# Kernel tuning notes

Hardware: AMD Instinct MI355X
Metric: run time of the kernel (lower is better)

Reference implementation:

```python
import jax, jax.numpy as jnp
import numpy as np

HEADS = 16
HIDDEN = 1024
DH = HIDDEN // HEADS
EPS = 1e-6


def setup_inputs() -> dict:
    key = jax.random.key(0)
    ks = jax.random.split(key, 18)
    B, S, D, H = 8, 4096, HIDDEN, HEADS
    std = 0.02
    inp = {
        "x": jax.random.normal(ks[0], (B, S, D), dtype=jnp.float32),
        "mask": jnp.zeros((B, 1, S), dtype=jnp.float32),
        "Wq": std * jax.random.normal(ks[1], (D, D), dtype=jnp.float32),
        "bq": jnp.zeros((D,), jnp.float32),
        "Wk": std * jax.random.normal(ks[2], (D, D), dtype=jnp.float32),
        "bk": jnp.zeros((D,), jnp.float32),
        "Wv": std * jax.random.normal(ks[3], (D, D), dtype=jnp.float32),
        "bv": jnp.zeros((D,), jnp.float32),
        "Wa": std * jax.random.normal(ks[4], (D, H), dtype=jnp.float32),
        "ba": jnp.zeros((H,), jnp.float32),
        "Wb": std * jax.random.normal(ks[5], (D, H), dtype=jnp.float32),
        "bb": jnp.zeros((H,), jnp.float32),
        "Wu": std * jax.random.normal(ks[6], (D, D), dtype=jnp.float32),
        "bu": jnp.zeros((D,), jnp.float32),
        "Wo": std * jax.random.normal(ks[7], (D, D), dtype=jnp.float32),
        "bo": jnp.zeros((D,), jnp.float32),
        "ln_g": jnp.ones((D,), jnp.float32),
        "ln_b": jnp.zeros((D,), jnp.float32),
    }
    return inp


def reference(x, mask, Wq, bq, Wk, bk, Wv, bv, Wa, ba, Wb, bb, Wu, bu, Wo, bo, ln_g, ln_b):
    B, S, D = x.shape
    H, dh = HEADS, D // HEADS
    scale = (D / H) ** -0.5

    q = x @ Wq + bq  # [B,S,D]
    k = x @ Wk + bk
    v = x @ Wv + bv

    # alpha pooling of q
    ascore = jnp.swapaxes((q @ Wa + ba) * scale, 1, 2) + mask  # [B,H,S]
    aw = jax.nn.softmax(ascore, axis=-1)
    qh = q.reshape(B, S, H, dh)
    q_av = jnp.einsum("bhs,bshd->bhd", aw, qh).reshape(B, 1, D)  # global query

    p = k * q_av  # [B,S,D], broadcast over seq

    # beta pooling of p
    bscore = jnp.swapaxes((p @ Wb + bb) * scale, 1, 2) + mask  # [B,H,S]
    bw = jax.nn.softmax(bscore, axis=-1)
    ph = p.reshape(B, S, H, dh)
    p_av = jnp.einsum("bhs,bshd->bhd", bw, ph).reshape(B, 1, D)  # global key

    u = p_av * v  # [B,S,D]
    r = u @ Wu + bu
    attn_out = (r + q) @ Wo + bo

    y = x + attn_out  # residual (dropout is identity at inference)
    mu = jnp.mean(y, axis=-1, keepdims=True)
    var = jnp.mean(jnp.square(y - mu), axis=-1, keepdims=True)
    return (y - mu) * jax.lax.rsqrt(var + EPS) * ln_g + ln_b
```

## Files before the change

### kernel.cpp

```cpp
#include <hip/hip_runtime.h>

typedef unsigned short u16;
typedef __bf16 bf16x8 __attribute__((ext_vector_type(8)));
typedef float  f32x4  __attribute__((ext_vector_type(4)));

__device__ __forceinline__ float b2f(u16 u) {
    unsigned int v = ((unsigned int)u) << 16;
    return __builtin_bit_cast(float, v);
}
__device__ __forceinline__ u16 f2b(float f) {
    unsigned int v = __builtin_bit_cast(unsigned int, f);
    v += 0x7fffu + ((v >> 16) & 1u);
    return (u16)(v >> 16);
}

#define GLD16(gp, lp) __builtin_amdgcn_global_load_lds( \
    (const __attribute__((address_space(1))) void*)(gp), \
    (__attribute__((address_space(3))) void*)(lp), 16, 0, 0)


__global__ __launch_bounds__(256) void convert_x(const float* __restrict__ x,
                                                 u16* __restrict__ xb) {
    size_t i = ((size_t)blockIdx.x * 256 + threadIdx.x) * 8;
    float4 v0 = *(const float4*)(x + i);
    float4 v1 = *(const float4*)(x + i + 4);
    ushort4 o0, o1;
    o0.x = f2b(v0.x); o0.y = f2b(v0.y); o0.z = f2b(v0.z); o0.w = f2b(v0.w);
    o1.x = f2b(v1.x); o1.y = f2b(v1.y); o1.z = f2b(v1.z); o1.w = f2b(v1.w);
    *(ushort4*)(xb + i)     = o0;
    *(ushort4*)(xb + i + 4) = o1;
}

__global__ __launch_bounds__(256) void transpose_w(const float* __restrict__ W,
                                                   u16* __restrict__ Wt) {
    __shared__ float tile[64][65];
    int kt = (blockIdx.x & 15) * 64;
    int nt = (blockIdx.x >> 4) * 64;
    int tid = threadIdx.x;
    int r = tid >> 4, c4 = (tid & 15) * 4;
    #pragma unroll
    for (int p = 0; p < 4; ++p) {
        int k = kt + p * 16 + r;
        float4 v = *(const float4*)(W + (size_t)k * 1024 + nt + c4);
        tile[c4 + 0][p * 16 + r] = v.x;
        tile[c4 + 1][p * 16 + r] = v.y;
        tile[c4 + 2][p * 16 + r] = v.z;
        tile[c4 + 3][p * 16 + r] = v.w;
    }
    __syncthreads();
    #pragma unroll
    for (int p = 0; p < 4; ++p) {
        int nl = p * 16 + r;
        ushort4 o;
        o.x = f2b(tile[nl][c4 + 0]); o.y = f2b(tile[nl][c4 + 1]);
        o.z = f2b(tile[nl][c4 + 2]); o.w = f2b(tile[nl][c4 + 3]);
        *(ushort4*)(Wt + (size_t)(nt + nl) * 1024 + kt + c4) = o;
    }
}

__global__ __launch_bounds__(256) void wu_prime(const float* __restrict__ Wu,
                                                const float* __restrict__ p_av,
                                                u16* __restrict__ Wut) {
    __shared__ float tile[64][65];
    int kt = (blockIdx.x & 15) * 64;
    int nt = (blockIdx.x >> 4) * 64;
    int tid = threadIdx.x;
    int r = tid >> 4, c4 = (tid & 15) * 4;
    #pragma unroll
    for (int p = 0; p < 4; ++p) {
        int k = kt + p * 16 + r;
        float4 v = *(const float4*)(Wu + (size_t)k * 1024 + nt + c4);
        tile[c4 + 0][p * 16 + r] = v.x;
        tile[c4 + 1][p * 16 + r] = v.y;
        tile[c4 + 2][p * 16 + r] = v.z;
        tile[c4 + 3][p * 16 + r] = v.w;
    }
    __syncthreads();
    for (int b = 0; b < 8; ++b) {
        float4 pv = *(const float4*)(p_av + (size_t)b * 1024 + kt + c4);
        #pragma unroll
        for (int p = 0; p < 4; ++p) {
            int nl = p * 16 + r;
            ushort4 o;
            o.x = f2b(tile[nl][c4 + 0] * pv.x);
            o.y = f2b(tile[nl][c4 + 1] * pv.y);
            o.z = f2b(tile[nl][c4 + 2] * pv.z);
            o.w = f2b(tile[nl][c4 + 3] * pv.w);
            *(ushort4*)(Wut + ((size_t)b * 1024 + nt + nl) * 1024 + kt + c4) = o;
        }
    }
}

__global__ __launch_bounds__(256) void wat_prep(const float* __restrict__ Wa,
                                                u16* __restrict__ Wat) {
    int idx = blockIdx.x * 256 + threadIdx.x;
    int h = idx >> 10, k = idx & 1023;
    Wat[idx] = f2b(Wa[(k << 4) + h]);
}

__global__ __launch_bounds__(256) void wbt_prep(const float* __restrict__ Wb,
                                                const float* __restrict__ q_av,
                                                u16* __restrict__ Wbt) {
    int idx = blockIdx.x * 256 + threadIdx.x;
    int b = idx >> 14, rem = idx & 16383;
    int h = rem >> 10, k = rem & 1023;
    Wbt[idx] = f2b(Wb[(k << 4) + h] * q_av[(b << 10) + k]);
}

__global__ __launch_bounds__(256) void bias_concat(const float* __restrict__ bq,
                                                   const float* __restrict__ bk,
                                                   const float* __restrict__ bv,
                                                   float* __restrict__ outb) {
    int i = blockIdx.x * 256 + threadIdx.x;
    outb[i] = (i < 1024) ? bq[i] : (i < 2048 ? bk[i - 1024] : bv[i - 2048]);
}

__global__ __launch_bounds__(256, 4)
void gemm_bf16(const u16* __restrict__ A, int lda,
               const u16* __restrict__ Bt,
               const float* __restrict__ bias,
               const u16* __restrict__ addsrc, int ldadd,
               u16* __restrict__ C, int ldc,
               int N, int K, int batch_rows) {
    __shared__ u16 As[128 * 64];
    __shared__ u16 Bs[128 * 64];
    int ntiles = N >> 7;
    int bid = blockIdx.x;
    int mtiles = gridDim.x / ntiles;
    int tm, tn;
    if ((mtiles & 7) == 0) {
        int xcd = bid & 7, s = bid >> 3;
        int mper = mtiles >> 3;
        tm = xcd * mper + s / ntiles;
        tn = s - (s / ntiles) * ntiles;
    } else {
        tm = bid / ntiles; tn = bid - (bid / ntiles) * ntiles;
    }
    int m0 = tm << 7, n0 = tn << 7;
    if (batch_rows > 0) Bt += (size_t)(m0 / batch_rows) * (size_t)N * K;
    int tid = threadIdx.x, lane = tid & 63, w = tid >> 6;
    int wm = (w >> 1) << 6, wn = (w & 1) << 6;
    int quad = lane >> 4, l16 = lane & 15;
    int rph = l16 & 7;
    int lrow = lane >> 3;
    int lkg  = (lane & 7) ^ lrow;

    int idxA = (m0 + (w << 5) + lrow) * lda + (lkg << 3);
    int idxB = (n0 + (w << 5) + lrow) * K   + (lkg << 3);
    int stepA = lda << 3, stepB = K << 3;

    f32x4 zero = {0.f, 0.f, 0.f, 0.f};
    f32x4 acc[4][4];
    #pragma unroll
    for (int i = 0; i < 4; ++i)
        #pragma unroll
        for (int j = 0; j < 4; ++j) acc[i][j] = zero;

    for (int kt = 0; kt < K; kt += 64) {
        __syncthreads();
        #pragma unroll
        for (int j = 0; j < 4; ++j) {
            int c = (w << 2) + j;
            GLD16(A  + (idxA + j * stepA + kt), &As[c << 9]);
            GLD16(Bt + (idxB + j * stepB + kt), &Bs[c << 9]);
        }
        __syncthreads();
        #pragma unroll
        for (int kk = 0; kk < 2; ++kk) {
            bf16x8 a[4], b[4];
            int kg = (((kk << 2) + quad) ^ rph) << 3;
            #pragma unroll
            for (int i = 0; i < 4; ++i) {
                a[i] = *(const bf16x8*)&As[((wm + (i << 4) + l16) << 6) + kg];
                b[i] = *(const bf16x8*)&Bs[((wn + (i << 4) + l16) << 6) + kg];
            }
            #pragma unroll
            for (int mi = 0; mi < 4; ++mi)
                #pragma unroll
                for (int ni = 0; ni < 4; ++ni)
                    acc[mi][ni] = __builtin_amdgcn_mfma_f32_16x16x32_bf16(
                        a[mi], b[ni], acc[mi][ni], 0, 0, 0);
        }
    }
    #pragma unroll
    for (int mi = 0; mi < 4; ++mi) {
        #pragma unroll
        for (int ni = 0; ni < 4; ++ni) {
            int col = n0 + wn + (ni << 4) + l16;
            float bv = bias[col];
            #pragma unroll
            for (int rg = 0; rg < 4; ++rg) {
                int rowg = m0 + wm + (mi << 4) + (quad << 2) + rg;
                float vv = acc[mi][ni][rg] + bv;
                if (addsrc) vv += b2f(addsrc[(size_t)rowg * ldadd + col]);
                C[(size_t)rowg * ldc + col] = f2b(vv);
            }
        }
    }
}

__global__ __launch_bounds__(256)
void score_gemm(const u16* __restrict__ A, int lda,
                const u16* __restrict__ Bt,
                const float* __restrict__ bias16,
                const float* __restrict__ mask,
                float* __restrict__ outsc,
                int batched) {
    __shared__ u16 As[256 * 64];
    __shared__ u16 Bs[16 * 64];
    int m0 = blockIdx.x << 8;
    int tid = threadIdx.x, lane = tid & 63, w = tid >> 6;
    int quad = lane >> 4, l16 = lane & 15;
    int rph = l16 & 7;
    int lrow = lane >> 3;
    int lkg  = (lane & 7) ^ lrow;
    const u16* Bb = Bt + (batched ? ((size_t)(m0 >> 12) << 14) : 0);

    int idxA = (m0 + (w << 6) + lrow) * lda + (lkg << 3);
    int stepA = lda << 3;
    int idxB = lrow * 1024 + (lkg << 3);

    f32x4 acc4[4];
    #pragma unroll
    for (int i = 0; i < 4; ++i) acc4[i] = (f32x4){0.f, 0.f, 0.f, 0.f};

    for (int kt = 0; kt < 1024; kt += 64) {
        __syncthreads();
        #pragma unroll
        for (int j = 0; j < 8; ++j) {
            int c = (w << 3) + j;
            GLD16(A + (idxA + j * stepA + kt), &As[c << 9]);
        }
        if (w < 2)
            GLD16(Bb + (idxB + w * 8192 + kt), &Bs[w << 9]);
        __syncthreads();
        #pragma unroll
        for (int kk = 0; kk < 2; ++kk) {
            int kg = (((kk << 2) + quad) ^ rph) << 3;
            bf16x8 b = *(const bf16x8*)&Bs[(l16 << 6) + kg];
            #pragma unroll
            for (int mi = 0; mi < 4; ++mi) {
                bf16x8 a = *(const bf16x8*)&As[(((w << 6) + (mi << 4) + l16) << 6) + kg];
                acc4[mi] = __builtin_amdgcn_mfma_f32_16x16x32_bf16(a, b, acc4[mi], 0, 0, 0);
            }
        }
    }
    int bidx = m0 >> 12;
    float bv = bias16[l16];
    float* orow = outsc + (((size_t)bidx << 4) + l16) * 4096;
    const float* mrow = mask + ((size_t)bidx << 12);
    #pragma unroll
    for (int mi = 0; mi < 4; ++mi) {
        int sbase = (m0 & 4095) + (w << 6) + (mi << 4) + (quad << 2);
        #pragma unroll
        for (int rg = 0; rg < 4; ++rg)
            orow[sbase + rg] = 0.125f * (acc4[mi][rg] + bv) + mrow[sbase + rg];
    }
}

__global__ __launch_bounds__(256)
void pool_kernel(const float* __restrict__ score,
                 const u16* __restrict__ X, int ldx,
                 const float* __restrict__ mulvec,
                 float* __restrict__ outav) {
    __shared__ float wbuf[4096];
    __shared__ float red[4];
    __shared__ float psum[16][64];
    int b = blockIdx.x >> 4, h = blockIdx.x & 15;
    int tid = threadIdx.x, lane = tid & 63, w = tid >> 6;
    const float* srow = score + (((size_t)b << 4) + h) * 4096;
    float mx = -1e30f;
    for (int s = tid; s < 4096; s += 256) mx = fmaxf(mx, srow[s]);
    for (int o = 32; o; o >>= 1) mx = fmaxf(mx, __shfl_xor(mx, o));
    if (lane == 0) red[w] = mx;
    __syncthreads();
    mx = fmaxf(fmaxf(red[0], red[1]), fmaxf(red[2], red[3]));
    __syncthreads();
    float sm = 0.f;
    for (int s = tid; s < 4096; s += 256) {
        float e = __expf(srow[s] - mx);
        wbuf[s] = e;
        sm += e;
    }
    for (int o = 32; o; o >>= 1) sm += __shfl_xor(sm, o);
    if (lane == 0) red[w] = sm;
    __syncthreads();
    float inv = 1.f / (red[0] + red[1] + red[2] + red[3]);
    int dg = (tid & 15) << 2;
    int sc = tid >> 4;
    const u16* base = X + ((size_t)(b << 12)) * ldx + (h << 6) + dg;
    float a0 = 0, a1 = 0, a2 = 0, a3 = 0;
    for (int s = sc << 8; s < (sc << 8) + 256; ++s) {
        float wv = wbuf[s];
        ushort4 uv = *(const ushort4*)(base + (size_t)s * ldx);
        a0 += wv * b2f(uv.x); a1 += wv * b2f(uv.y);
        a2 += wv * b2f(uv.z); a3 += wv * b2f(uv.w);
    }
    psum[sc][dg + 0] = a0; psum[sc][dg + 1] = a1;
    psum[sc][dg + 2] = a2; psum[sc][dg + 3] = a3;
    __syncthreads();
    if (tid < 64) {
        float t = 0.f;
        #pragma unroll
        for (int j = 0; j < 16; ++j) t += psum[j][tid];
        t *= inv;
        if (mulvec) t *= mulvec[((size_t)b << 10) + (h << 6) + tid];
        outav[((size_t)b << 10) + (h << 6) + tid] = t;
    }
}

__global__ __launch_bounds__(256)
void ln_kernel(const u16* __restrict__ Z, const float* __restrict__ g,
               const float* __restrict__ bta, float* __restrict__ outp) {
    __shared__ float rs1[4], rs2[4];
    int row = blockIdx.x, tid = threadIdx.x;
    const u16* zr = Z + ((size_t)row << 10);
    ushort4 uv = *(const ushort4*)(zr + (tid << 2));
    float v0 = b2f(uv.x), v1 = b2f(uv.y), v2 = b2f(uv.z), v3 = b2f(uv.w);
    float s = v0 + v1 + v2 + v3;
    float s2 = v0 * v0 + v1 * v1 + v2 * v2 + v3 * v3;
    for (int o = 32; o; o >>= 1) { s += __shfl_xor(s, o); s2 += __shfl_xor(s2, o); }
    if ((tid & 63) == 0) { rs1[tid >> 6] = s; rs2[tid >> 6] = s2; }
    __syncthreads();
    float S = rs1[0] + rs1[1] + rs1[2] + rs1[3];
    float S2 = rs2[0] + rs2[1] + rs2[2] + rs2[3];
    float mean = S * (1.0f / 1024.0f);
    float var = S2 * (1.0f / 1024.0f) - mean * mean;
    float inv = rsqrtf(var + 1e-6f);
    int c = tid << 2;
    float4 o4;
    o4.x = (v0 - mean) * inv * g[c + 0] + bta[c + 0];
    o4.y = (v1 - mean) * inv * g[c + 1] + bta[c + 1];
    o4.z = (v2 - mean) * inv * g[c + 2] + bta[c + 2];
    o4.w = (v3 - mean) * inv * g[c + 3] + bta[c + 3];
    *(float4*)(outp + ((size_t)row << 10) + c) = o4;
}


extern "C" void kernel_launch(void* const* d_in, const int* in_sizes, int n_in,
                              void* d_out, int out_size, void* d_ws, size_t ws_size,
                              hipStream_t stream) {
    (void)in_sizes; (void)n_in; (void)out_size;
    const float* x    = (const float*)d_in[0];
    const float* mask = (const float*)d_in[1];
    const float* Wq   = (const float*)d_in[2];
    const float* bq   = (const float*)d_in[3];
    const float* Wk   = (const float*)d_in[4];
    const float* bk   = (const float*)d_in[5];
    const float* Wv   = (const float*)d_in[6];
    const float* bv   = (const float*)d_in[7];
    const float* Wa   = (const float*)d_in[8];
    const float* ba   = (const float*)d_in[9];
    const float* Wb   = (const float*)d_in[10];
    const float* bb   = (const float*)d_in[11];
    const float* Wu   = (const float*)d_in[12];
    const float* bu   = (const float*)d_in[13];
    const float* Wo   = (const float*)d_in[14];
    const float* bo   = (const float*)d_in[15];
    const float* ln_g = (const float*)d_in[16];
    const float* ln_b = (const float*)d_in[17];
    float* outp = (float*)d_out;

    char* ws = (char*)d_ws;
    u16*   xb    = (u16*)(ws);
    u16*   qkv   = (u16*)(ws + 67108864);
    u16*   Wqkvt = (u16*)(ws + 268435456);
    u16*   Wot   = (u16*)(ws + 274726912);
    u16*   Wat   = (u16*)(ws + 276824064);
    u16*   Wbt   = (u16*)(ws + 276856832);
    float* score = (float*)(ws + 277118976);
    float* q_av  = (float*)(ws + 279216128);
    float* p_av  = (float*)(ws + 279248896);
    float* biasq = (float*)(ws + 279281664);
    u16*   Wubt  = (u16*)(ws + 279293952);
    if (ws_size < 296071168ULL) return;

    convert_x<<<16384, 256, 0, stream>>>(x, xb);
    transpose_w<<<256, 256, 0, stream>>>(Wq, Wqkvt);
    transpose_w<<<256, 256, 0, stream>>>(Wk, Wqkvt + 1048576);
    transpose_w<<<256, 256, 0, stream>>>(Wv, Wqkvt + 2097152);
    transpose_w<<<256, 256, 0, stream>>>(Wo, Wot);
    wat_prep<<<64, 256, 0, stream>>>(Wa, Wat);
    bias_concat<<<12, 256, 0, stream>>>(bq, bk, bv, biasq);

    gemm_bf16<<<6144, 256, 0, stream>>>(xb, 1024, Wqkvt, biasq,
                                        nullptr, 0, qkv, 3072, 3072, 1024, 0);
    score_gemm<<<128, 256, 0, stream>>>(qkv, 3072, Wat, ba, mask, score, 0);
    pool_kernel<<<128, 256, 0, stream>>>(score, qkv, 3072, nullptr, q_av);
    wbt_prep<<<512, 256, 0, stream>>>(Wb, q_av, Wbt);
    score_gemm<<<128, 256, 0, stream>>>(qkv + 1024, 3072, Wbt, bb, mask, score, 1);
    pool_kernel<<<128, 256, 0, stream>>>(score, qkv + 1024, 3072, q_av, p_av);
    wu_prime<<<256, 256, 0, stream>>>(Wu, p_av, Wubt);
    gemm_bf16<<<2048, 256, 0, stream>>>(qkv + 2048, 3072, Wubt, bu,
                                        qkv, 3072, qkv, 3072, 1024, 1024, 4096);
    gemm_bf16<<<2048, 256, 0, stream>>>(qkv, 3072, Wot, bo,
                                        xb, 1024, xb, 1024, 1024, 1024, 0);
    ln_kernel<<<32768, 256, 0, stream>>>(xb, ln_g, ln_b, outp);
}
```

Measured before the change: 871.6 us.

## Rewrite bf16 GEMM with 256x256 tiles and triple-buffered LDS prefetch pipeline

The GEMM kernel moves from 128x128 tiles with 256 threads to 256x256 tiles with 512 threads (8 waves, each computing a 128x64 sub-tile). The K loop becomes a triple-buffered pipeline over 32-wide K slices. Global-to-LDS loads for slice t+2 are issued between two MFMA half-phases, with fine-grained waitcnt and barriers and s_setprio raised around the MFMA blocks. This is meant to raise data reuse per loaded byte and hide memory latency behind compute. The cost is 96KB of LDS per block, more accumulator registers and lower occupancy.

```diff
diff --git a/kernel.cpp b/kernel.cpp
--- a/kernel.cpp
+++ b/kernel.cpp
@@ -115,16 +115,15 @@
     outb[i] = (i < 1024) ? bq[i] : (i < 2048 ? bk[i - 1024] : bv[i - 2048]);
 }
 
-__global__ __launch_bounds__(256, 4)
+__global__ __launch_bounds__(512, 2)
 void gemm_bf16(const u16* __restrict__ A, int lda,
                const u16* __restrict__ Bt,
                const float* __restrict__ bias,
                const u16* __restrict__ addsrc, int ldadd,
                u16* __restrict__ C, int ldc,
                int N, int K, int batch_rows) {
-    __shared__ u16 As[128 * 64];
-    __shared__ u16 Bs[128 * 64];
-    int ntiles = N >> 7;
+    __shared__ u16 lds[3 * 16384];
+    int ntiles = N >> 8;
     int bid = blockIdx.x;
     int mtiles = gridDim.x / ntiles;
     int tm, tn;
@@ -136,61 +135,108 @@
     } else {
         tm = bid / ntiles; tn = bid - (bid / ntiles) * ntiles;
     }
-    int m0 = tm << 7, n0 = tn << 7;
+    int m0 = tm << 8, n0 = tn << 8;
     if (batch_rows > 0) Bt += (size_t)(m0 / batch_rows) * (size_t)N * K;
     int tid = threadIdx.x, lane = tid & 63, w = tid >> 6;
-    int wm = (w >> 1) << 6, wn = (w & 1) << 6;
+    int wm = w >> 2, wn = w & 3;
     int quad = lane >> 4, l16 = lane & 15;
-    int rph = l16 & 7;
-    int lrow = lane >> 3;
-    int lkg  = (lane & 7) ^ lrow;
-
-    int idxA = (m0 + (w << 5) + lrow) * lda + (lkg << 3);
-    int idxB = (n0 + (w << 5) + lrow) * K   + (lkg << 3);
-    int stepA = lda << 3, stepB = K << 3;
+
+    int srow = (w << 5) + (lane >> 2);
+    int sk = ((lane & 3) ^ ((lane >> 3) & 3)) << 3;
+    const u16* Asrc = A  + (size_t)(m0 + srow) * lda + sk;
+    const u16* Bsrc = Bt + (size_t)(n0 + srow) * K   + sk;
+    int ldst = w << 10;
+    int astep = lda << 4, bstep = K << 4;
+
+    int swz = (quad ^ ((l16 >> 1) & 3)) << 3;
+    int aoff = (((wm << 7) + l16) << 5) + swz;
+    int boff = (((wn << 6) + l16) << 5) + swz + 8192;
+    int nt = K >> 5;
 
     f32x4 zero = {0.f, 0.f, 0.f, 0.f};
-    f32x4 acc[4][4];
-    #pragma unroll
-    for (int i = 0; i < 4; ++i)
+    f32x4 acc[8][4];
+    #pragma unroll
+    for (int i = 0; i < 8; ++i)
         #pragma unroll
         for (int j = 0; j < 4; ++j) acc[i][j] = zero;
 
-    for (int kt = 0; kt < K; kt += 64) {
-        __syncthreads();
-        #pragma unroll
-        for (int j = 0; j < 4; ++j) {
-            int c = (w << 2) + j;
-            GLD16(A  + (idxA + j * stepA + kt), &As[c << 9]);
-            GLD16(Bt + (idxB + j * stepB + kt), &Bs[c << 9]);
-        }
-        __syncthreads();
-        #pragma unroll
-        for (int kk = 0; kk < 2; ++kk) {
-            bf16x8 a[4], b[4];
-            int kg = (((kk << 2) + quad) ^ rph) << 3;
+    GLD16(Asrc,                &lds[ldst]);
+    GLD16(Asrc + astep,        &lds[ldst + 512]);
+    GLD16(Bsrc,                &lds[8192 + ldst]);
+    GLD16(Bsrc + bstep,        &lds[8192 + ldst + 512]);
+    GLD16(Asrc + 32,           &lds[16384 + ldst]);
+    GLD16(Asrc + astep + 32,   &lds[16384 + ldst + 512]);
+    GLD16(Bsrc + 32,           &lds[16384 + 8192 + ldst]);
+    GLD16(Bsrc + bstep + 32,   &lds[16384 + 8192 + ldst + 512]);
+    asm volatile("s_waitcnt vmcnt(4)" ::: "memory");
+    __builtin_amdgcn_s_barrier();
+
+    int bufc = 0;
+    int koff = 64;
+    for (int t = 0; t < nt; ++t) {
+        const u16* Lc = lds + (bufc << 14);
+        int bufs = bufc + 2; if (bufs >= 3) bufs -= 3;
+        u16* Ls = lds + (bufs << 14);
+        bool pf = (t + 2 < nt);
+
+        bf16x8 bfr[4], afr[4];
+        #pragma unroll
+        for (int ni = 0; ni < 4; ++ni)
+            bfr[ni] = *(const bf16x8*)&Lc[boff + (ni << 9)];
+        #pragma unroll
+        for (int mi = 0; mi < 4; ++mi)
+            afr[mi] = *(const bf16x8*)&Lc[aoff + (mi << 9)];
+        if (pf) {
+            GLD16(Asrc + koff,         &Ls[ldst]);
+            GLD16(Asrc + astep + koff, &Ls[ldst + 512]);
+        }
+        asm volatile("" ::: "memory");
+        __builtin_amdgcn_s_barrier();
+        __builtin_amdgcn_s_setprio(1);
+        #pragma unroll
+        for (int mi = 0; mi < 4; ++mi)
             #pragma unroll
-            for (int i = 0; i < 4; ++i) {
-                a[i] = *(const bf16x8*)&As[((wm + (i << 4) + l16) << 6) + kg];
-                b[i] = *(const bf16x8*)&Bs[((wn + (i << 4) + l16) << 6) + kg];
-            }
+            for (int ni = 0; ni < 4; ++ni)
+                acc[mi][ni] = __builtin_amdgcn_mfma_f32_16x16x32_bf16(
+                    afr[mi], bfr[ni], acc[mi][ni], 0, 0, 0);
+        __builtin_amdgcn_s_setprio(0);
+        asm volatile("" ::: "memory");
+        __builtin_amdgcn_s_barrier();
+
+        #pragma unroll
+        for (int mi = 0; mi < 4; ++mi)
+            afr[mi] = *(const bf16x8*)&Lc[aoff + ((mi + 4) << 9)];
+        if (pf) {
+            GLD16(Bsrc + koff,         &Ls[8192 + ldst]);
+            GLD16(Bsrc + bstep + koff, &Ls[8192 + ldst + 512]);
+        }
+        asm volatile("" ::: "memory");
+        __builtin_amdgcn_s_barrier();
+        __builtin_amdgcn_s_setprio(1);
+        #pragma unroll
+        for (int mi = 0; mi < 4; ++mi)
             #pragma unroll
-            for (int mi = 0; mi < 4; ++mi)
-                #pragma unroll
-                for (int ni = 0; ni < 4; ++ni)
-                    acc[mi][ni] = __builtin_amdgcn_mfma_f32_16x16x32_bf16(
-                        a[mi], b[ni], acc[mi][ni], 0, 0, 0);
-        }
-    }
-    #pragma unroll
-    for (int mi = 0; mi < 4; ++mi) {
+            for (int ni = 0; ni < 4; ++ni)
+                acc[mi + 4][ni] = __builtin_amdgcn_mfma_f32_16x16x32_bf16(
+                    afr[mi], bfr[ni], acc[mi + 4][ni], 0, 0, 0);
+        __builtin_amdgcn_s_setprio(0);
+        if (pf) asm volatile("s_waitcnt vmcnt(4)" ::: "memory");
+        else    asm volatile("s_waitcnt vmcnt(0)" ::: "memory");
+        __builtin_amdgcn_s_barrier();
+
+        koff += 32;
+        bufc = (bufc == 2) ? 0 : bufc + 1;
+    }
+
+    #pragma unroll
+    for (int mi = 0; mi < 8; ++mi) {
         #pragma unroll
         for (int ni = 0; ni < 4; ++ni) {
-            int col = n0 + wn + (ni << 4) + l16;
+            int col = n0 + (wn << 6) + (ni << 4) + l16;
             float bv = bias[col];
             #pragma unroll
             for (int rg = 0; rg < 4; ++rg) {
-                int rowg = m0 + wm + (mi << 4) + (quad << 2) + rg;
+                int rowg = m0 + (wm << 7) + (mi << 4) + (quad << 2) + rg;
                 float vv = acc[mi][ni][rg] + bv;
                 if (addsrc) vv += b2f(addsrc[(size_t)rowg * ldadd + col]);
                 C[(size_t)rowg * ldc + col] = f2b(vv);
@@ -383,7 +429,7 @@
     wat_prep<<<64, 256, 0, stream>>>(Wa, Wat);
     bias_concat<<<12, 256, 0, stream>>>(bq, bk, bv, biasq);
 
-    gemm_bf16<<<6144, 256, 0, stream>>>(xb, 1024, Wqkvt, biasq,
+    gemm_bf16<<<1536, 512, 0, stream>>>(xb, 1024, Wqkvt, biasq,
                                         nullptr, 0, qkv, 3072, 3072, 1024, 0);
     score_gemm<<<128, 256, 0, stream>>>(qkv, 3072, Wat, ba, mask, score, 0);
     pool_kernel<<<128, 256, 0, stream>>>(score, qkv, 3072, nullptr, q_av);
@@ -391,9 +437,9 @@
     score_gemm<<<128, 256, 0, stream>>>(qkv + 1024, 3072, Wbt, bb, mask, score, 1);
     pool_kernel<<<128, 256, 0, stream>>>(score, qkv + 1024, 3072, q_av, p_av);
     wu_prime<<<256, 256, 0, stream>>>(Wu, p_av, Wubt);
-    gemm_bf16<<<2048, 256, 0, stream>>>(qkv + 2048, 3072, Wubt, bu,
-                                        qkv, 3072, qkv, 3072, 1024, 1024, 4096);
-    gemm_bf16<<<2048, 256, 0, stream>>>(qkv, 3072, Wot, bo,
-                                        xb, 1024, xb, 1024, 1024, 1024, 0);
+    gemm_bf16<<<512, 512, 0, stream>>>(qkv + 2048, 3072, Wubt, bu,
+                                       qkv, 3072, qkv, 3072, 1024, 1024, 4096);
+    gemm_bf16<<<512, 512, 0, stream>>>(qkv, 3072, Wot, bo,
+                                       xb, 1024, xb, 1024, 1024, 1024, 0);
     ln_kernel<<<32768, 256, 0, stream>>>(xb, ln_g, ln_b, outp);
 }
```

New measurement: 928.1 us. 1.06x slower.

## Split score GEMM into smaller tiles and parallelise pooling across sequence chunks

Applied to the files above, without the earlier changes.

The score GEMM now uses 64-row tiles instead of 256, launching 512 blocks rather than 128 so more of the GPU's compute units get work. The fused softmax-and-pool kernel is split into three steps: a softmax kernel that writes normalised weights back in place, a pool_sum kernel that handles 8 sequence chunks per (batch, head) across 1024 blocks, and a finalize kernel that reduces the partial sums and applies the multiplier. This targets the low occupancy of the previous 128-block kernels. The cost is extra kernel launches, an extra pass over the score buffer in global memory, and a partial-sum buffer.

```diff
diff --git a/kernel.cpp b/kernel.cpp
--- a/kernel.cpp
+++ b/kernel.cpp
@@ -206,9 +206,9 @@
                 const float* __restrict__ mask,
                 float* __restrict__ outsc,
                 int batched) {
-    __shared__ u16 As[256 * 64];
+    __shared__ u16 As[64 * 64];
     __shared__ u16 Bs[16 * 64];
-    int m0 = blockIdx.x << 8;
+    int m0 = blockIdx.x << 6;
     int tid = threadIdx.x, lane = tid & 63, w = tid >> 6;
     int quad = lane >> 4, l16 = lane & 15;
     int rph = l16 & 7;
@@ -216,19 +216,17 @@
     int lkg  = (lane & 7) ^ lrow;
     const u16* Bb = Bt + (batched ? ((size_t)(m0 >> 12) << 14) : 0);
 
-    int idxA = (m0 + (w << 6) + lrow) * lda + (lkg << 3);
+    int idxA = (m0 + (w << 4) + lrow) * lda + (lkg << 3);
     int stepA = lda << 3;
     int idxB = lrow * 1024 + (lkg << 3);
 
-    f32x4 acc4[4];
-    #pragma unroll
-    for (int i = 0; i < 4; ++i) acc4[i] = (f32x4){0.f, 0.f, 0.f, 0.f};
+    f32x4 acc4 = (f32x4){0.f, 0.f, 0.f, 0.f};
 
     for (int kt = 0; kt < 1024; kt += 64) {
         __syncthreads();
         #pragma unroll
-        for (int j = 0; j < 8; ++j) {
-            int c = (w << 3) + j;
+        for (int j = 0; j < 2; ++j) {
+            int c = (w << 1) + j;
             GLD16(A + (idxA + j * stepA + kt), &As[c << 9]);
         }
         if (w < 2)
@@ -238,37 +236,26 @@
         for (int kk = 0; kk < 2; ++kk) {
             int kg = (((kk << 2) + quad) ^ rph) << 3;
             bf16x8 b = *(const bf16x8*)&Bs[(l16 << 6) + kg];
-            #pragma unroll
-            for (int mi = 0; mi < 4; ++mi) {
-                bf16x8 a = *(const bf16x8*)&As[(((w << 6) + (mi << 4) + l16) << 6) + kg];
-                acc4[mi] = __builtin_amdgcn_mfma_f32_16x16x32_bf16(a, b, acc4[mi], 0, 0, 0);
-            }
+            bf16x8 a = *(const bf16x8*)&As[(((w << 4) + l16) << 6) + kg];
+            acc4 = __builtin_amdgcn_mfma_f32_16x16x32_bf16(a, b, acc4, 0, 0, 0);
         }
     }
     int bidx = m0 >> 12;
     float bv = bias16[l16];
     float* orow = outsc + (((size_t)bidx << 4) + l16) * 4096;
     const float* mrow = mask + ((size_t)bidx << 12);
-    #pragma unroll
-    for (int mi = 0; mi < 4; ++mi) {
-        int sbase = (m0 & 4095) + (w << 6) + (mi << 4) + (quad << 2);
-        #pragma unroll
-        for (int rg = 0; rg < 4; ++rg)
-            orow[sbase + rg] = 0.125f * (acc4[mi][rg] + bv) + mrow[sbase + rg];
-    }
+    int sbase = (m0 & 4095) + (w << 4) + (quad << 2);
+    #pragma unroll
+    for (int rg = 0; rg < 4; ++rg)
+        orow[sbase + rg] = 0.125f * (acc4[rg] + bv) + mrow[sbase + rg];
 }
 
 __global__ __launch_bounds__(256)
-void pool_kernel(const float* __restrict__ score,
-                 const u16* __restrict__ X, int ldx,
-                 const float* __restrict__ mulvec,
-                 float* __restrict__ outav) {
+void softmax_kernel(float* __restrict__ score) {
     __shared__ float wbuf[4096];
     __shared__ float red[4];
-    __shared__ float psum[16][64];
-    int b = blockIdx.x >> 4, h = blockIdx.x & 15;
     int tid = threadIdx.x, lane = tid & 63, w = tid >> 6;
-    const float* srow = score + (((size_t)b << 4) + h) * 4096;
+    float* srow = score + (size_t)blockIdx.x * 4096;
     float mx = -1e30f;
     for (int s = tid; s < 4096; s += 256) mx = fmaxf(mx, srow[s]);
     for (int o = 32; o; o >>= 1) mx = fmaxf(mx, __shfl_xor(mx, o));
@@ -286,12 +273,24 @@
     if (lane == 0) red[w] = sm;
     __syncthreads();
     float inv = 1.f / (red[0] + red[1] + red[2] + red[3]);
+    for (int s = tid; s < 4096; s += 256) srow[s] = wbuf[s] * inv;
+}
+
+__global__ __launch_bounds__(256)
+void pool_sum(const float* __restrict__ wn,
+              const u16* __restrict__ X, int ldx,
+              float* __restrict__ part) {
+    __shared__ float psum[16][64];
+    int blk = blockIdx.x, tid = threadIdx.x;
+    int cc = blk & 7, bh = blk >> 3;
+    int b = bh >> 4, h = bh & 15;
+    const float* wrow = wn + ((size_t)bh << 12) + (cc << 9);
     int dg = (tid & 15) << 2;
     int sc = tid >> 4;
-    const u16* base = X + ((size_t)(b << 12)) * ldx + (h << 6) + dg;
+    const u16* base = X + (size_t)((b << 12) + (cc << 9) + (sc << 5)) * ldx + (h << 6) + dg;
     float a0 = 0, a1 = 0, a2 = 0, a3 = 0;
-    for (int s = sc << 8; s < (sc << 8) + 256; ++s) {
-        float wv = wbuf[s];
+    for (int s = 0; s < 32; ++s) {
+        float wv = wrow[(sc << 5) + s];
         ushort4 uv = *(const ushort4*)(base + (size_t)s * ldx);
         a0 += wv * b2f(uv.x); a1 += wv * b2f(uv.y);
         a2 += wv * b2f(uv.z); a3 += wv * b2f(uv.w);
@@ -303,10 +302,21 @@
         float t = 0.f;
         #pragma unroll
         for (int j = 0; j < 16; ++j) t += psum[j][tid];
-        t *= inv;
-        if (mulvec) t *= mulvec[((size_t)b << 10) + (h << 6) + tid];
-        outav[((size_t)b << 10) + (h << 6) + tid] = t;
-    }
+        part[(((size_t)bh << 3) + cc) * 64 + tid] = t;
+    }
+}
+
+__global__ __launch_bounds__(256)
+void pool_finalize(const float* __restrict__ part,
+                   const float* __restrict__ mul,
+                   float* __restrict__ outav) {
+    int idx = blockIdx.x * 256 + threadIdx.x;
+    const float* p = part + ((size_t)(idx >> 6) << 9) + (idx & 63);
+    float s = 0.f;
+    #pragma unroll
+    for (int c = 0; c < 8; ++c) s += p[c << 6];
+    if (mul) s *= mul[idx];
+    outav[idx] = s;
 }
 
 __global__ __launch_bounds__(256)
@@ -373,7 +383,8 @@
     float* p_av  = (float*)(ws + 279248896);
     float* biasq = (float*)(ws + 279281664);
     u16*   Wubt  = (u16*)(ws + 279293952);
-    if (ws_size < 296071168ULL) return;
+    float* part  = (float*)(ws + 296071168);
+    if (ws_size < 296333312ULL) return;
 
     convert_x<<<16384, 256, 0, stream>>>(x, xb);
     transpose_w<<<256, 256, 0, stream>>>(Wq, Wqkvt);
@@ -385,11 +396,15 @@
 
     gemm_bf16<<<6144, 256, 0, stream>>>(xb, 1024, Wqkvt, biasq,
                                         nullptr, 0, qkv, 3072, 3072, 1024, 0);
-    score_gemm<<<128, 256, 0, stream>>>(qkv, 3072, Wat, ba, mask, score, 0);
-    pool_kernel<<<128, 256, 0, stream>>>(score, qkv, 3072, nullptr, q_av);
+    score_gemm<<<512, 256, 0, stream>>>(qkv, 3072, Wat, ba, mask, score, 0);
+    softmax_kernel<<<128, 256, 0, stream>>>(score);
+    pool_sum<<<1024, 256, 0, stream>>>(score, qkv, 3072, part);
+    pool_finalize<<<32, 256, 0, stream>>>(part, nullptr, q_av);
     wbt_prep<<<512, 256, 0, stream>>>(Wb, q_av, Wbt);
-    score_gemm<<<128, 256, 0, stream>>>(qkv + 1024, 3072, Wbt, bb, mask, score, 1);
-    pool_kernel<<<128, 256, 0, stream>>>(score, qkv + 1024, 3072, q_av, p_av);
+    score_gemm<<<512, 256, 0, stream>>>(qkv + 1024, 3072, Wbt, bb, mask, score, 1);
+    softmax_kernel<<<128, 256, 0, stream>>>(score);
+    pool_sum<<<1024, 256, 0, stream>>>(score, qkv + 1024, 3072, part);
+    pool_finalize<<<32, 256, 0, stream>>>(part, q_av, p_av);
     wu_prime<<<256, 256, 0, stream>>>(Wu, p_av, Wubt);
     gemm_bf16<<<2048, 256, 0, stream>>>(qkv + 2048, 3072, Wubt, bu,
                                         qkv, 3072, qkv, 3072, 1024, 1024, 4096);
```

New measurement: 850.3 us. 2.4% less time.
